# Performance work log

Measured on AMD Instinct MI355X. Metric: run time of the kernel, lower is better.

## Reference

```python
import jax, jax.numpy as jnp
import numpy as np

C, H, W = 3, 224, 224
P = 14  # patches per row
PS = H // P  # 16
PATCH_DIM = C * PS * PS  # 768
HIDDEN = 768


def patchify(images):
    # images: [n, c, h, w] -> [n, P*P, c*PS*PS], flatten order (c, ph, pw)
    n = images.shape[0]
    x = images.reshape(n, C, P, PS, P, PS)
    x = x.transpose(0, 2, 4, 1, 3, 5)  # [n, Pi, Pj, c, ps, ps]
    return x.reshape(n, P * P, PATCH_DIM)


def setup_inputs() -> dict:
    key = jax.random.key(0)
    k1, k2, k3 = jax.random.split(key, 3)
    images = jax.random.normal(k1, (128, C, H, W), dtype=jnp.float32)
    # nn.Linear(patch_embedding_dim, hidden_dim): weight [out, in], bias [out]
    bound = 1.0 / np.sqrt(PATCH_DIM)
    W_lin = jax.random.uniform(k2, (HIDDEN, PATCH_DIM), minval=-bound, maxval=bound, dtype=jnp.float32)
    b_lin = jax.random.uniform(k3, (HIDDEN,), minval=-bound, maxval=bound, dtype=jnp.float32)
    cls_token = jnp.ones((1, HIDDEN), dtype=jnp.float32)
    return {"images": images, "W_lin": W_lin, "b_lin": b_lin, "cls_token": cls_token}


def reference(images, W_lin, b_lin, cls_token):
    patches = patchify(images)                        # [n, 196, 768]
    hidden = jnp.einsum('npd,hd->nph', patches, W_lin) + b_lin  # [n, 196, H]
    n = images.shape[0]
    cls = jnp.broadcast_to(cls_token[None], (n, 1, HIDDEN))
    return jnp.concatenate([cls, hidden], axis=1)     # [n, 197, H]
```

## Files before the change

kernel.cpp:

```cpp
#include <hip/hip_runtime.h>
#include <cstdint>


#define PGRID 14
#define PSZ   16
#define CHN   3
#define IMGW  224
#define KDIM  768
#define NDIM  768
#define NPATCH 196

typedef short bf16x8 __attribute__((ext_vector_type(8)));
typedef short short8v __attribute__((ext_vector_type(8)));
typedef float f32x4  __attribute__((ext_vector_type(4)));

__device__ __forceinline__ short bf16rne(float f) {
    uint32_t u = __builtin_bit_cast(uint32_t, f);
    u += 0x7FFFu + ((u >> 16) & 1u);
    return (short)(u >> 16);
}

__device__ __forceinline__ short8v cvt8(float4 v0, float4 v1) {
    short8v s;
    s[0] = bf16rne(v0.x); s[1] = bf16rne(v0.y); s[2] = bf16rne(v0.z); s[3] = bf16rne(v0.w);
    s[4] = bf16rne(v1.x); s[5] = bf16rne(v1.y); s[6] = bf16rne(v1.z); s[7] = bf16rne(v1.w);
    return s;
}

__global__ __launch_bounds__(256) void prep_all(
    const float* __restrict__ img, const float* __restrict__ Wl,
    const float* __restrict__ cls, short* __restrict__ A,
    short* __restrict__ Wb, float* __restrict__ out, int n_img)
{
    const int IMG8 = n_img * (CHN * IMGW * IMGW / 8);
    const int W8   = KDIM * NDIM / 8;
    int t = blockIdx.x * 256 + threadIdx.x;

    if (t < IMG8) {
        int w8    = t % (IMGW / 8);
        int rest  = t / (IMGW / 8);
        int h     = rest % IMGW;
        int rest2 = rest / IMGW;
        int c     = rest2 % CHN;
        int im    = rest2 / CHN;

        float4 v0 = *(const float4*)(img + (long)t * 8);
        float4 v1 = *(const float4*)(img + (long)t * 8 + 4);

        int Pi = h >> 4;
        int ph = h & 15;
        int Pj = w8 >> 1;
        int pw = (w8 & 1) * 8;
        int m  = im * NPATCH + Pi * PGRID + Pj;
        int k  = (c << 8) + (ph << 4) + pw;
        *(short8v*)(A + (long)m * KDIM + k) = cvt8(v0, v1);
    } else if (t < IMG8 + W8) {
        int u = t - IMG8;
        float4 v0 = *(const float4*)(Wl + (long)u * 8);
        float4 v1 = *(const float4*)(Wl + (long)u * 8 + 4);
        *(short8v*)(Wb + (long)u * 8) = cvt8(v0, v1);
    } else {
        int u = t - IMG8 - W8;
        if (u < n_img * (NDIM / 8)) {
            int im = u / (NDIM / 8);
            int k8 = u - im * (NDIM / 8);
            float4 v0 = *(const float4*)(cls + k8 * 8);
            float4 v1 = *(const float4*)(cls + k8 * 8 + 4);
            float* dst = out + (long)im * 197 * NDIM + k8 * 8;
            *(float4*)dst = v0;
            *(float4*)(dst + 4) = v1;
        }
    }
}

__global__ __launch_bounds__(256) void vit_gemm3(
    const short* __restrict__ A, const short* __restrict__ B,
    const float* __restrict__ bias, float* __restrict__ out,
    int M, int mgroups)
{
    const int bid = blockIdx.x;
    const int xcd = bid & 7;
    const int s   = bid >> 3;
    const int gq  = s / 6;
    const int j   = s - gq * 6;
    const int g   = gq * 8 + xcd;
    if (g >= mgroups) return;
    const int m0 = g * 128;
    const int n0 = j * 128;

    __shared__ short As0[128 * 64];
    __shared__ short Bs0[128 * 64];
    __shared__ short As1[128 * 64];
    __shared__ short Bs1[128 * 64];

    const int tid = threadIdx.x;
    const int wave = tid >> 6;
    const int lane = tid & 63;

    const int srow = tid >> 3;
    const int sk   = (tid & 7) ^ (srow & 7);
    const long abase = (long)(m0 + srow) * KDIM + sk * 8;
    const long bbase = (long)(n0 + srow) * KDIM + sk * 8;

    const int wm = (wave & 1) * 64;
    const int wn = (wave >> 1) * 64;
    const int wq = lane >> 4;
    const int lr = lane & 15;
    const int blk0 = ((wq)     ^ (lr & 7)) * 8;
    const int blk1 = ((wq + 4) ^ (lr & 7)) * 8;

    f32x4 acc[4][4] = {};
    bf16x8 sa0[4], sb0[4], sa1[4], sb1[4];

#define LOADT(SA, SB, KOFF)                                                  \
    {                                                                        \
        _Pragma("unroll")                                                    \
        for (int jj = 0; jj < 4; ++jj) {                                     \
            SA[jj] = *(const bf16x8*)(A + abase + (long)jj * 32 * KDIM + (KOFF)); \
            SB[jj] = *(const bf16x8*)(B + bbase + (long)jj * 32 * KDIM + (KOFF)); \
        }                                                                    \
    }

#define WRITET(AS, BS, SA, SB)                                               \
    {                                                                        \
        _Pragma("unroll")                                                    \
        for (int jj = 0; jj < 4; ++jj) {                                     \
            *(bf16x8*)(&AS[(jj * 256 + tid) * 8]) = SA[jj];                  \
            *(bf16x8*)(&BS[(jj * 256 + tid) * 8]) = SB[jj];                  \
        }                                                                    \
    }

#define COMPUTE(AS, BS)                                                      \
    {                                                                        \
        _Pragma("unroll")                                                    \
        for (int ks = 0; ks < 2; ++ks) {                                     \
            const int blk = ks ? blk1 : blk0;                                \
            bf16x8 a[4], b[4];                                               \
            _Pragma("unroll")                                                \
            for (int i = 0; i < 4; ++i)                                      \
                a[i] = *(const bf16x8*)(&AS[(wm + i * 16 + lr) * 64 + blk]); \
            _Pragma("unroll")                                                \
            for (int i = 0; i < 4; ++i)                                      \
                b[i] = *(const bf16x8*)(&BS[(wn + i * 16 + lr) * 64 + blk]); \
            _Pragma("unroll")                                                \
            for (int i = 0; i < 4; ++i)                                      \
                _Pragma("unroll")                                            \
                for (int jm = 0; jm < 4; ++jm)                               \
                    acc[i][jm] = __builtin_amdgcn_mfma_f32_16x16x32_bf16(    \
                        a[i], b[jm], acc[i][jm], 0, 0, 0);                   \
        }                                                                    \
    }

    LOADT(sa0, sb0, 0)
    LOADT(sa1, sb1, 64)
    WRITET(As0, Bs0, sa0, sb0)
    __syncthreads();

    #pragma unroll
    for (int u = 0; u < 6; ++u) {
        const int t = 2 * u;
        if (t + 1 < 12) WRITET(As1, Bs1, sa1, sb1)
        if (t + 2 < 12) LOADT(sa0, sb0, (t + 2) * 64)
        COMPUTE(As0, Bs0)
        __syncthreads();
        if (t + 2 < 12) WRITET(As0, Bs0, sa0, sb0)
        if (t + 3 < 12) LOADT(sa1, sb1, (t + 3) * 64)
        COMPUTE(As1, Bs1)
        __syncthreads();
    }

#undef LOADT
#undef WRITET
#undef COMPUTE

    float bv[4];
    #pragma unroll
    for (int jm = 0; jm < 4; ++jm) bv[jm] = bias[n0 + wn + jm * 16 + lr];

    #pragma unroll
    for (int i = 0; i < 4; ++i) {
        #pragma unroll
        for (int r = 0; r < 4; ++r) {
            int gm = m0 + wm + i * 16 + wq * 4 + r;
            if (gm < M) {
                int im = gm / NPATCH;
                int p  = gm - im * NPATCH;
                long orow = ((long)im * 197 + 1 + p) * (long)NDIM;
                #pragma unroll
                for (int jm = 0; jm < 4; ++jm)
                    out[orow + n0 + wn + jm * 16 + lr] = acc[i][jm][r] + bv[jm];
            }
        }
    }
}

#define LDSTR 40
__global__ __launch_bounds__(256) void vit_gemm_fb(
    const float* __restrict__ img, const float* __restrict__ Wl,
    const float* __restrict__ bias, float* __restrict__ out, int n_img)
{
    const int M = n_img * NPATCH;
    __shared__ short As[128 * LDSTR];
    __shared__ short Bs[128 * LDSTR];
    const int tid = threadIdx.x;
    const int m0 = blockIdx.y * 128;
    const int n0 = blockIdx.x * 128;
    const int col4  = tid & 7;
    const int rbase = tid >> 3;
    long arow[4];
    for (int rr = 0; rr < 4; ++rr) {
        int m = m0 + rbase + rr * 32;
        int mm = (m < M) ? m : (M - 1);
        int im = mm / NPATCH;
        int p  = mm % NPATCH;
        int Pi = p / PGRID;
        int Pj = p % PGRID;
        arow[rr] = ((long)(im * CHN) * IMGW + Pi * PSZ) * IMGW + Pj * PSZ;
    }
    const int lane = tid & 63;
    const int wave = tid >> 6;
    const int wm = (wave & 1) * 64;
    const int wn = (wave >> 1) * 64;
    const int wq = lane >> 4;
    const int lr = lane & 15;
    f32x4 acc[4][4] = {};
    for (int k0 = 0; k0 < KDIM; k0 += 32) {
        {
            int k  = k0 + col4 * 4;
            int c  = k >> 8;
            int ph = (k >> 4) & 15;
            int pw = k & 15;
            long koff = (long)(c * IMGW + ph) * IMGW + pw;
            #pragma unroll
            for (int rr = 0; rr < 4; ++rr) {
                const float4 v = *(const float4*)(img + arow[rr] + koff);
                int row = rbase + rr * 32;
                short4 s;
                s.x = bf16rne(v.x); s.y = bf16rne(v.y);
                s.z = bf16rne(v.z); s.w = bf16rne(v.w);
                *(short4*)(&As[row * LDSTR + col4 * 4]) = s;
            }
        }
        {
            int k = k0 + col4 * 4;
            #pragma unroll
            for (int rr = 0; rr < 4; ++rr) {
                int nrow = rbase + rr * 32;
                const float4 v = *(const float4*)(Wl + (long)(n0 + nrow) * KDIM + k);
                short4 s;
                s.x = bf16rne(v.x); s.y = bf16rne(v.y);
                s.z = bf16rne(v.z); s.w = bf16rne(v.w);
                *(short4*)(&Bs[nrow * LDSTR + col4 * 4]) = s;
            }
        }
        __syncthreads();
        bf16x8 a[4], b[4];
        #pragma unroll
        for (int i = 0; i < 4; ++i)
            a[i] = *(const bf16x8*)(&As[(wm + i * 16 + lr) * LDSTR + wq * 8]);
        #pragma unroll
        for (int i = 0; i < 4; ++i)
            b[i] = *(const bf16x8*)(&Bs[(wn + i * 16 + lr) * LDSTR + wq * 8]);
        #pragma unroll
        for (int i = 0; i < 4; ++i)
            #pragma unroll
            for (int j = 0; j < 4; ++j)
                acc[i][j] = __builtin_amdgcn_mfma_f32_16x16x32_bf16(a[i], b[j], acc[i][j], 0, 0, 0);
        __syncthreads();
    }
    float bv[4];
    #pragma unroll
    for (int j = 0; j < 4; ++j) bv[j] = bias[n0 + wn + j * 16 + lr];
    #pragma unroll
    for (int i = 0; i < 4; ++i) {
        #pragma unroll
        for (int r = 0; r < 4; ++r) {
            int gm = m0 + wm + i * 16 + wq * 4 + r;
            if (gm < M) {
                int im = gm / NPATCH;
                int p  = gm % NPATCH;
                long orow = ((long)im * 197 + 1 + p) * (long)NDIM;
                #pragma unroll
                for (int j = 0; j < 4; ++j)
                    out[orow + n0 + wn + j * 16 + lr] = acc[i][j][r] + bv[j];
            }
        }
    }
}

__global__ __launch_bounds__(256) void cls_fill(
    const float* __restrict__ cls, float* __restrict__ out, int n_img)
{
    int i = blockIdx.x * 256 + threadIdx.x;
    if (i < n_img * NDIM) {
        int im = i / NDIM;
        int n  = i - im * NDIM;
        out[(long)im * 197 * NDIM + n] = cls[n];
    }
}

extern "C" void kernel_launch(void* const* d_in, const int* in_sizes, int n_in,
                              void* d_out, int out_size, void* d_ws, size_t ws_size,
                              hipStream_t stream) {
    const float* img  = (const float*)d_in[0];
    const float* Wl   = (const float*)d_in[1];
    const float* bias = (const float*)d_in[2];
    const float* cls  = (const float*)d_in[3];
    float* out = (float*)d_out;

    int n_img = in_sizes[0] / (CHN * IMGW * IMGW);
    int M = n_img * NPATCH;
    int mgroups = (M + 127) / 128;
    long Mpad = (long)mgroups * 128;

    size_t need = (size_t)(Mpad * KDIM + (long)KDIM * NDIM) * sizeof(short);
    if (ws_size >= need) {
        short* A_ws = (short*)d_ws;
        short* Wb   = A_ws + Mpad * KDIM;

        int total8 = n_img * (CHN * IMGW * IMGW / 8)
                   + KDIM * NDIM / 8
                   + n_img * (NDIM / 8);
        prep_all<<<(total8 + 255) / 256, 256, 0, stream>>>(img, Wl, cls, A_ws, Wb, out, n_img);

        int gpad = (mgroups + 7) & ~7;
        int nblocks = gpad * 6;
        vit_gemm3<<<nblocks, 256, 0, stream>>>(A_ws, Wb, bias, out, M, mgroups);
    } else {
        dim3 grid(NDIM / 128, mgroups);
        vit_gemm_fb<<<grid, 256, 0, stream>>>(img, Wl, bias, out, n_img);
        int cls_elems = n_img * NDIM;
        cls_fill<<<(cls_elems + 255) / 256, 256, 0, stream>>>(cls, out, n_img);
    }
}
```

Measured before the change: 174.8 us.

## Enlarge GEMM tiles to 256x256 with direct global-to-LDS async loads

Replaces the 128x128, 256-thread GEMM with a 256x256, 512-thread kernel. Tiles are staged through global_load_lds straight into double-buffered LDS, with explicit vmcnt waits and barriers instead of a register round trip, and blocks are remapped so each XCD gets a contiguous range. The goal is more operand reuse per tile and less VGPR and instruction overhead from staging. In exchange it uses 128KB of LDS per block, gets one block per CU, and leaves fewer workgroups to cover the machine, which can hurt occupancy and tail balance.

```diff
diff --git a/kernel.cpp b/kernel.cpp
--- a/kernel.cpp
+++ b/kernel.cpp
@@ -13,6 +13,13 @@
 typedef short bf16x8 __attribute__((ext_vector_type(8)));
 typedef short short8v __attribute__((ext_vector_type(8)));
 typedef float f32x4  __attribute__((ext_vector_type(4)));
+
+typedef __attribute__((address_space(1))) void GV;
+typedef __attribute__((address_space(3))) void LV;
+
+__device__ __forceinline__ void gload_lds16(const void* g, void* l) {
+    __builtin_amdgcn_global_load_lds((GV*)g, (LV*)l, 16, 0, 0);
+}
 
 __device__ __forceinline__ short bf16rne(float f) {
     uint32_t u = __builtin_bit_cast(uint32_t, f);
@@ -73,77 +80,68 @@
     }
 }
 
-__global__ __launch_bounds__(256) void vit_gemm3(
+__global__ __launch_bounds__(512) void vit_gemm4(
     const short* __restrict__ A, const short* __restrict__ B,
     const float* __restrict__ bias, float* __restrict__ out,
     int M, int mgroups)
 {
-    const int bid = blockIdx.x;
-    const int xcd = bid & 7;
-    const int s   = bid >> 3;
-    const int gq  = s / 6;
-    const int j   = s - gq * 6;
-    const int g   = gq * 8 + xcd;
-    if (g >= mgroups) return;
-    const int m0 = g * 128;
-    const int n0 = j * 128;
-
-    __shared__ short As0[128 * 64];
-    __shared__ short Bs0[128 * 64];
-    __shared__ short As1[128 * 64];
-    __shared__ short Bs1[128 * 64];
-
-    const int tid = threadIdx.x;
-    const int wave = tid >> 6;
+    const int nwg = mgroups * 3;
+    const int q = nwg >> 3, r = nwg & 7;
+    const int xcd = blockIdx.x & 7;
+    const int idx = blockIdx.x >> 3;
+    const int wgid = (xcd < r ? xcd * (q + 1) : r * (q + 1) + (xcd - r) * q) + idx;
+    const int g = wgid / 3;
+    const int j = wgid - g * 3;
+    const int m0 = g * 256;
+    const int n0 = j * 256;
+
+    __shared__ short LDS[2][32768];
+
+    const int tid  = threadIdx.x;
+    const int wid  = tid >> 6;
     const int lane = tid & 63;
+    const int wr = wid >> 2;
+    const int wc = wid & 3;
+    const int wm = wr * 128;
+    const int wn = wc * 64;
+    const int wq = lane >> 4;
+    const int lr = lane & 15;
+    const int blk0 = ((wq)     ^ (lr & 7)) * 8;
+    const int blk1 = ((wq + 4) ^ (lr & 7)) * 8;
 
     const int srow = tid >> 3;
     const int sk   = (tid & 7) ^ (srow & 7);
     const long abase = (long)(m0 + srow) * KDIM + sk * 8;
     const long bbase = (long)(n0 + srow) * KDIM + sk * 8;
-
-    const int wm = (wave & 1) * 64;
-    const int wn = (wave >> 1) * 64;
-    const int wq = lane >> 4;
-    const int lr = lane & 15;
-    const int blk0 = ((wq)     ^ (lr & 7)) * 8;
-    const int blk1 = ((wq + 4) ^ (lr & 7)) * 8;
-
-    f32x4 acc[4][4] = {};
-    bf16x8 sa0[4], sb0[4], sa1[4], sb1[4];
-
-#define LOADT(SA, SB, KOFF)                                                  \
+    const int  lslot = tid * 8;
+
+    f32x4 acc[8][4] = {};
+
+#define STAGE(CUR, KK)                                                       \
     {                                                                        \
         _Pragma("unroll")                                                    \
-        for (int jj = 0; jj < 4; ++jj) {                                     \
-            SA[jj] = *(const bf16x8*)(A + abase + (long)jj * 32 * KDIM + (KOFF)); \
-            SB[jj] = *(const bf16x8*)(B + bbase + (long)jj * 32 * KDIM + (KOFF)); \
+        for (int l = 0; l < 4; ++l) {                                        \
+            gload_lds16(A + abase + (long)l * 64 * KDIM + (KK),              \
+                        &LDS[CUR][l * 4096 + lslot]);                        \
+            gload_lds16(B + bbase + (long)l * 64 * KDIM + (KK),              \
+                        &LDS[CUR][16384 + l * 4096 + lslot]);                \
         }                                                                    \
     }
 
-#define WRITET(AS, BS, SA, SB)                                               \
-    {                                                                        \
-        _Pragma("unroll")                                                    \
-        for (int jj = 0; jj < 4; ++jj) {                                     \
-            *(bf16x8*)(&AS[(jj * 256 + tid) * 8]) = SA[jj];                  \
-            *(bf16x8*)(&BS[(jj * 256 + tid) * 8]) = SB[jj];                  \
-        }                                                                    \
-    }
-
-#define COMPUTE(AS, BS)                                                      \
+#define COMPUTE(CUR)                                                         \
     {                                                                        \
         _Pragma("unroll")                                                    \
         for (int ks = 0; ks < 2; ++ks) {                                     \
             const int blk = ks ? blk1 : blk0;                                \
-            bf16x8 a[4], b[4];                                               \
+            bf16x8 a[8], b[4];                                               \
             _Pragma("unroll")                                                \
-            for (int i = 0; i < 4; ++i)                                      \
-                a[i] = *(const bf16x8*)(&AS[(wm + i * 16 + lr) * 64 + blk]); \
+            for (int i = 0; i < 8; ++i)                                      \
+                a[i] = *(const bf16x8*)(&LDS[CUR][(wm + i * 16 + lr) * 64 + blk]); \
             _Pragma("unroll")                                                \
-            for (int i = 0; i < 4; ++i)                                      \
-                b[i] = *(const bf16x8*)(&BS[(wn + i * 16 + lr) * 64 + blk]); \
+            for (int jm = 0; jm < 4; ++jm)                                   \
+                b[jm] = *(const bf16x8*)(&LDS[CUR][16384 + (wn + jm * 16 + lr) * 64 + blk]); \
             _Pragma("unroll")                                                \
-            for (int i = 0; i < 4; ++i)                                      \
+            for (int i = 0; i < 8; ++i)                                      \
                 _Pragma("unroll")                                            \
                 for (int jm = 0; jm < 4; ++jm)                               \
                     acc[i][jm] = __builtin_amdgcn_mfma_f32_16x16x32_bf16(    \
@@ -151,26 +149,23 @@
         }                                                                    \
     }
 
-    LOADT(sa0, sb0, 0)
-    LOADT(sa1, sb1, 64)
-    WRITET(As0, Bs0, sa0, sb0)
-    __syncthreads();
-
-    #pragma unroll
-    for (int u = 0; u < 6; ++u) {
-        const int t = 2 * u;
-        if (t + 1 < 12) WRITET(As1, Bs1, sa1, sb1)
-        if (t + 2 < 12) LOADT(sa0, sb0, (t + 2) * 64)
-        COMPUTE(As0, Bs0)
-        __syncthreads();
-        if (t + 2 < 12) WRITET(As0, Bs0, sa0, sb0)
-        if (t + 3 < 12) LOADT(sa1, sb1, (t + 3) * 64)
-        COMPUTE(As1, Bs1)
-        __syncthreads();
-    }
-
-#undef LOADT
-#undef WRITET
+    STAGE(0, 0)
+    STAGE(1, 64)
+
+    for (int t = 0; t < 12; ++t) {
+        const int cur = t & 1;
+        if (t == 11) { asm volatile("s_waitcnt vmcnt(0)" ::: "memory"); }
+        else         { asm volatile("s_waitcnt vmcnt(8)" ::: "memory"); }
+        __builtin_amdgcn_s_barrier();
+        asm volatile("" ::: "memory");
+        COMPUTE(cur)
+        asm volatile("" ::: "memory");
+        __builtin_amdgcn_s_barrier();
+        asm volatile("" ::: "memory");
+        if (t < 10) STAGE(cur, (t + 2) * 64)
+    }
+
+#undef STAGE
 #undef COMPUTE
 
     float bv[4];
@@ -178,17 +173,17 @@
     for (int jm = 0; jm < 4; ++jm) bv[jm] = bias[n0 + wn + jm * 16 + lr];
 
     #pragma unroll
-    for (int i = 0; i < 4; ++i) {
-        #pragma unroll
-        for (int r = 0; r < 4; ++r) {
-            int gm = m0 + wm + i * 16 + wq * 4 + r;
+    for (int i = 0; i < 8; ++i) {
+        #pragma unroll
+        for (int rr = 0; rr < 4; ++rr) {
+            int gm = m0 + wm + i * 16 + wq * 4 + rr;
             if (gm < M) {
                 int im = gm / NPATCH;
                 int p  = gm - im * NPATCH;
                 long orow = ((long)im * 197 + 1 + p) * (long)NDIM;
                 #pragma unroll
                 for (int jm = 0; jm < 4; ++jm)
-                    out[orow + n0 + wn + jm * 16 + lr] = acc[i][jm][r] + bv[jm];
+                    out[orow + n0 + wn + jm * 16 + lr] = acc[i][jm][rr] + bv[jm];
             }
         }
     }
@@ -310,8 +305,8 @@
 
     int n_img = in_sizes[0] / (CHN * IMGW * IMGW);
     int M = n_img * NPATCH;
-    int mgroups = (M + 127) / 128;
-    long Mpad = (long)mgroups * 128;
+    int mgroups = (M + 255) / 256;
+    long Mpad = (long)mgroups * 256;
 
     size_t need = (size_t)(Mpad * KDIM + (long)KDIM * NDIM) * sizeof(short);
     if (ws_size >= need) {
@@ -323,11 +318,10 @@
                    + n_img * (NDIM / 8);
         prep_all<<<(total8 + 255) / 256, 256, 0, stream>>>(img, Wl, cls, A_ws, Wb, out, n_img);
 
-        int gpad = (mgroups + 7) & ~7;
-        int nblocks = gpad * 6;
-        vit_gemm3<<<nblocks, 256, 0, stream>>>(A_ws, Wb, bias, out, M, mgroups);
+        int nwg = mgroups * 3;
+        vit_gemm4<<<nwg, 512, 0, stream>>>(A_ws, Wb, bias, out, M, mgroups);
     } else {
-        dim3 grid(NDIM / 128, mgroups);
+        dim3 grid(NDIM / 128, (M + 127) / 128);
         vit_gemm_fb<<<grid, 256, 0, stream>>>(img, Wl, bias, out, n_img);
         int cls_elems = n_img * NDIM;
         cls_fill<<<(cls_elems + 255) / 256, 256, 0, stream>>>(cls, out, n_img);
```

After: 190.7 us. 1.09x slower.
